# Performance work log

Hardware: AMD Instinct MI355X
Metric: run time of the kernel (lower is better)

## Reference

```python
import jax, jax.numpy as jnp
import numpy as np

RES = 512
STEPS = 128
SIGMA = 0.01


def _sample_cubic(curves, t):
    # curves: [N,4,2], t: [S] in [0,1]. De Casteljau, matching the torch module.
    p0, p1, p2, p3 = curves[:, 0], curves[:, 1], curves[:, 2], curves[:, 3]  # each [N,2]

    def lerp(a, b):  # [N,2] -> [N,2,S]
        return a[:, :, None] + (b - a)[:, :, None] * t

    a01, a12, a23 = lerp(p0, p1), lerp(p1, p2), lerp(p2, p3)
    qa = a01 + t * (a12 - a01)   # quadratic over first 3 points
    qb = a12 + t * (a23 - a12)   # quadratic over last 3 points
    curve = qa + t * (qb - qa)   # cubic, [N,2,S]
    # torch.cat([...], dim=1) over curves of shape [2,S] -> [2, N*S]
    return jnp.moveaxis(curve, 0, 1).reshape(2, -1)


def setup_inputs() -> dict:
    key = jax.random.key(0)
    curves = jax.random.uniform(key, (8, 4, 2), dtype=jnp.float32)
    return {"curves": curves}


def reference(curves) -> jnp.ndarray:
    t = jnp.linspace(0.0, 1.0, STEPS)
    curve = _sample_cubic(curves, t)  # [2, T], T = N*STEPS
    x, y = curve[0], curve[1]
    grid = jnp.arange(RES, dtype=curve.dtype) / RES  # pixel coords / res
    inv = 1.0 / (2.0 * SIGMA * SIGMA)
    # exp(-(dx^2+dy^2)/2s^2) factors exactly: raster[a,b] = sum_s Ex[a,s]*Ey[b,s]
    Ex = jnp.exp(-(x[None, :] - grid[:, None]) ** 2 * inv)  # [RES, T]
    Ey = jnp.exp(-(y[None, :] - grid[:, None]) ** 2 * inv)  # [RES, T]
    raster = Ex @ Ey.T  # [RES, RES], raster[a,b]
    # torch returns transpose(raster, 0, 1)
    return raster.T
```

## Files before the change

### kernel.cpp

```cpp
#include <hip/hip_runtime.h>


constexpr int RES_   = 512;
constexpr int TILE   = 64;
constexpr int KSPLIT = 8;
constexpr int KB     = 1024 / KSPLIT;
constexpr int KC     = 64;

__global__ __launch_bounds__(256)
void bezier_partial(const float* __restrict__ curves, float* __restrict__ part) {
    __shared__ float xs[KB], ys[KB];
    __shared__ float ex_s[KC][TILE];
    __shared__ float ey_s[KC][TILE];

    const int tid   = threadIdx.x;
    const int ibase = blockIdx.x * TILE;
    const int jbase = blockIdx.y * TILE;
    const int kbase = blockIdx.z * KB;

    if (tid < KB) {
        int p = kbase + tid;
        int c = p >> 7;
        float t = (float)(p & 127) * (1.0f / 127.0f);
        const float* cp = curves + c * 8;
        float p0x = cp[0], p0y = cp[1];
        float p1x = cp[2], p1y = cp[3];
        float p2x = cp[4], p2y = cp[5];
        float p3x = cp[6], p3y = cp[7];
        float a01x = p0x + (p1x - p0x) * t, a01y = p0y + (p1y - p0y) * t;
        float a12x = p1x + (p2x - p1x) * t, a12y = p1y + (p2y - p1y) * t;
        float a23x = p2x + (p3x - p2x) * t, a23y = p2y + (p3y - p2y) * t;
        float qax = a01x + (a12x - a01x) * t, qay = a01y + (a12y - a01y) * t;
        float qbx = a12x + (a23x - a12x) * t, qby = a12y + (a23y - a12y) * t;
        xs[tid] = qax + (qbx - qax) * t;
        ys[tid] = qay + (qby - qay) * t;
    }
    __syncthreads();

    const int it = tid & 15, jt = tid >> 4;
    const int ib = it * 4, jb = jt * 4;
    float acc[4][4];
#pragma unroll
    for (int r = 0; r < 4; ++r)
#pragma unroll
        for (int c = 0; c < 4; ++c) acc[r][c] = 0.0f;

    for (int chunk = 0; chunk < KB / KC; ++chunk) {
#pragma unroll
        for (int e = 0; e < (KC * TILE) / 256; ++e) {
            int idx = e * 256 + tid;
            int kk  = idx >> 6;
            int ii  = idx & 63;
            float xv = xs[chunk * KC + kk];
            float yv = ys[chunk * KC + kk];
            float dx = xv - (float)(ibase + ii) * (1.0f / 512.0f);
            float dy = yv - (float)(jbase + ii) * (1.0f / 512.0f);
            ex_s[kk][ii] = __expf(dx * dx * (-5000.0f));
            ey_s[kk][ii] = __expf(dy * dy * (-5000.0f));
        }
        __syncthreads();

#pragma unroll 4
        for (int kk = 0; kk < KC; ++kk) {
            const float4 a = *reinterpret_cast<const float4*>(&ex_s[kk][ib]);
            const float4 b = *reinterpret_cast<const float4*>(&ey_s[kk][jb]);
            acc[0][0] += b.x * a.x; acc[0][1] += b.x * a.y;
            acc[0][2] += b.x * a.z; acc[0][3] += b.x * a.w;
            acc[1][0] += b.y * a.x; acc[1][1] += b.y * a.y;
            acc[1][2] += b.y * a.z; acc[1][3] += b.y * a.w;
            acc[2][0] += b.z * a.x; acc[2][1] += b.z * a.y;
            acc[2][2] += b.z * a.z; acc[2][3] += b.z * a.w;
            acc[3][0] += b.w * a.x; acc[3][1] += b.w * a.y;
            acc[3][2] += b.w * a.z; acc[3][3] += b.w * a.w;
        }
        __syncthreads();
    }

    float* slice = part + (size_t)blockIdx.z * (RES_ * RES_);
#pragma unroll
    for (int r = 0; r < 4; ++r) {
        int j = jbase + jb + r;
        float4 v = make_float4(acc[r][0], acc[r][1], acc[r][2], acc[r][3]);
        *reinterpret_cast<float4*>(&slice[j * RES_ + ibase + ib]) = v;
    }
}

__global__ __launch_bounds__(256)
void reduce_k(const float* __restrict__ part, float* __restrict__ out) {
    int i = blockIdx.x * blockDim.x + threadIdx.x;
    const float4* p4 = reinterpret_cast<const float4*>(part);
    float4 s = p4[i];
#pragma unroll
    for (int z = 1; z < KSPLIT; ++z) {
        float4 v = p4[(size_t)z * (RES_ * RES_ / 4) + i];
        s.x += v.x; s.y += v.y; s.z += v.z; s.w += v.w;
    }
    reinterpret_cast<float4*>(out)[i] = s;
}

extern "C" void kernel_launch(void* const* d_in, const int* in_sizes, int n_in,
                              void* d_out, int out_size, void* d_ws, size_t ws_size,
                              hipStream_t stream) {
    const float* curves = (const float*)d_in[0];
    float* out  = (float*)d_out;
    float* part = (float*)d_ws;

    dim3 grid(RES_ / TILE, RES_ / TILE, KSPLIT);
    bezier_partial<<<grid, dim3(256), 0, stream>>>(curves, part);

    reduce_k<<<dim3(RES_ * RES_ / 4 / 256), dim3(256), 0, stream>>>(part, out);
}
```

Baseline: 67.44 us.

## Use 128x128 tiles with 8x8 register blocking and 16-way K split

Each block now covers a 128x128 output tile, and each thread accumulates an 8x8 register tile instead of 4x4. The K split rises from 8 to 16, so each block handles 64 samples. All exp factors for those samples are computed once into shared memory, which drops the chunk loop and its extra barriers. This raises arithmetic intensity per shared-memory load, but it doubles the partial-sum buffer written by the first kernel and read by the reduction. It also halves the block count and needs 16 slices of workspace.

```diff
diff --git a/kernel.cpp b/kernel.cpp
--- a/kernel.cpp
+++ b/kernel.cpp
@@ -2,16 +2,15 @@
 
 
 constexpr int RES_   = 512;
-constexpr int TILE   = 64;
-constexpr int KSPLIT = 8;
+constexpr int TILE   = 128;
+constexpr int KSPLIT = 16;
 constexpr int KB     = 1024 / KSPLIT;
-constexpr int KC     = 64;
 
 __global__ __launch_bounds__(256)
 void bezier_partial(const float* __restrict__ curves, float* __restrict__ part) {
     __shared__ float xs[KB], ys[KB];
-    __shared__ float ex_s[KC][TILE];
-    __shared__ float ey_s[KC][TILE];
+    __shared__ float ex_s[KB][TILE];
+    __shared__ float ey_s[KB][TILE];
 
     const int tid   = threadIdx.x;
     const int ibase = blockIdx.x * TILE;
@@ -37,51 +36,50 @@
     }
     __syncthreads();
 
+#pragma unroll
+    for (int e = 0; e < (KB * TILE) / 256; ++e) {
+        int idx = e * 256 + tid;
+        int kk  = idx >> 7;
+        int ii  = idx & 127;
+        float xv = xs[kk];
+        float yv = ys[kk];
+        float dx = xv - (float)(ibase + ii) * (1.0f / 512.0f);
+        float dy = yv - (float)(jbase + ii) * (1.0f / 512.0f);
+        ex_s[kk][ii] = __expf(dx * dx * (-5000.0f));
+        ey_s[kk][ii] = __expf(dy * dy * (-5000.0f));
+    }
+    __syncthreads();
+
     const int it = tid & 15, jt = tid >> 4;
-    const int ib = it * 4, jb = jt * 4;
-    float acc[4][4];
+    const int ib = it * 8, jb = jt * 8;
+    float acc[8][8];
 #pragma unroll
-    for (int r = 0; r < 4; ++r)
+    for (int r = 0; r < 8; ++r)
 #pragma unroll
-        for (int c = 0; c < 4; ++c) acc[r][c] = 0.0f;
+        for (int c = 0; c < 8; ++c) acc[r][c] = 0.0f;
 
-    for (int chunk = 0; chunk < KB / KC; ++chunk) {
+#pragma unroll 2
+    for (int kk = 0; kk < KB; ++kk) {
+        const float4 a0 = *reinterpret_cast<const float4*>(&ex_s[kk][ib]);
+        const float4 a1 = *reinterpret_cast<const float4*>(&ex_s[kk][ib + 4]);
+        const float4 b0 = *reinterpret_cast<const float4*>(&ey_s[kk][jb]);
+        const float4 b1 = *reinterpret_cast<const float4*>(&ey_s[kk][jb + 4]);
+        const float av[8] = {a0.x, a0.y, a0.z, a0.w, a1.x, a1.y, a1.z, a1.w};
+        const float bv[8] = {b0.x, b0.y, b0.z, b0.w, b1.x, b1.y, b1.z, b1.w};
 #pragma unroll
-        for (int e = 0; e < (KC * TILE) / 256; ++e) {
-            int idx = e * 256 + tid;
-            int kk  = idx >> 6;
-            int ii  = idx & 63;
-            float xv = xs[chunk * KC + kk];
-            float yv = ys[chunk * KC + kk];
-            float dx = xv - (float)(ibase + ii) * (1.0f / 512.0f);
-            float dy = yv - (float)(jbase + ii) * (1.0f / 512.0f);
-            ex_s[kk][ii] = __expf(dx * dx * (-5000.0f));
-            ey_s[kk][ii] = __expf(dy * dy * (-5000.0f));
-        }
-        __syncthreads();
-
-#pragma unroll 4
-        for (int kk = 0; kk < KC; ++kk) {
-            const float4 a = *reinterpret_cast<const float4*>(&ex_s[kk][ib]);
-            const float4 b = *reinterpret_cast<const float4*>(&ey_s[kk][jb]);
-            acc[0][0] += b.x * a.x; acc[0][1] += b.x * a.y;
-            acc[0][2] += b.x * a.z; acc[0][3] += b.x * a.w;
-            acc[1][0] += b.y * a.x; acc[1][1] += b.y * a.y;
-            acc[1][2] += b.y * a.z; acc[1][3] += b.y * a.w;
-            acc[2][0] += b.z * a.x; acc[2][1] += b.z * a.y;
-            acc[2][2] += b.z * a.z; acc[2][3] += b.z * a.w;
-            acc[3][0] += b.w * a.x; acc[3][1] += b.w * a.y;
-            acc[3][2] += b.w * a.z; acc[3][3] += b.w * a.w;
-        }
-        __syncthreads();
+        for (int r = 0; r < 8; ++r)
+#pragma unroll
+            for (int c = 0; c < 8; ++c)
+                acc[r][c] += bv[r] * av[c];
     }
 
     float* slice = part + (size_t)blockIdx.z * (RES_ * RES_);
 #pragma unroll
-    for (int r = 0; r < 4; ++r) {
+    for (int r = 0; r < 8; ++r) {
         int j = jbase + jb + r;
-        float4 v = make_float4(acc[r][0], acc[r][1], acc[r][2], acc[r][3]);
-        *reinterpret_cast<float4*>(&slice[j * RES_ + ibase + ib]) = v;
+        float* row = &slice[j * RES_ + ibase + ib];
+        *reinterpret_cast<float4*>(row)     = make_float4(acc[r][0], acc[r][1], acc[r][2], acc[r][3]);
+        *reinterpret_cast<float4*>(row + 4) = make_float4(acc[r][4], acc[r][5], acc[r][6], acc[r][7]);
     }
 }
 
```

Result: slower. 73.63 us (+9.2%).

## Fuse split-K reduction into main kernel via last-block ticket counter

Applied to the files above, without the earlier changes.

Removes the separate reduction kernel. Each block writes its partial tile to a tile-contiguous workspace, then bumps a per-tile atomic ticket, and the last of the KSPLIT blocks sums the partials and writes the output tile. The Gaussian table fill is also vectorised so each thread computes four exps and does float4 shared stores. This trades a kernel launch and a full-image partial pass for a memset, threadfences and an atomic, and the final reduction now runs on only 64 blocks.

```diff
diff --git a/kernel.cpp b/kernel.cpp
--- a/kernel.cpp
+++ b/kernel.cpp
@@ -6,17 +6,21 @@
 constexpr int KSPLIT = 8;
 constexpr int KB     = 1024 / KSPLIT;
 constexpr int KC     = 64;
+constexpr int NTX    = RES_ / TILE;
 
 __global__ __launch_bounds__(256)
-void bezier_partial(const float* __restrict__ curves, float* __restrict__ part) {
+void bezier_fused(const float* __restrict__ curves, float* __restrict__ out,
+                  unsigned int* __restrict__ tickets, float* __restrict__ part) {
     __shared__ float xs[KB], ys[KB];
-    __shared__ float ex_s[KC][TILE];
-    __shared__ float ey_s[KC][TILE];
+    __shared__ __align__(16) float ex_s[KC][TILE];
+    __shared__ __align__(16) float ey_s[KC][TILE];
+    __shared__ unsigned int s_old;
 
-    const int tid   = threadIdx.x;
-    const int ibase = blockIdx.x * TILE;
-    const int jbase = blockIdx.y * TILE;
-    const int kbase = blockIdx.z * KB;
+    const int tid     = threadIdx.x;
+    const int ibase   = blockIdx.x * TILE;
+    const int jbase   = blockIdx.y * TILE;
+    const int tile_id = blockIdx.y * NTX + blockIdx.x;
+    const int kbase   = blockIdx.z * KB;
 
     if (tid < KB) {
         int p = kbase + tid;
@@ -47,16 +51,27 @@
 
     for (int chunk = 0; chunk < KB / KC; ++chunk) {
 #pragma unroll
-        for (int e = 0; e < (KC * TILE) / 256; ++e) {
-            int idx = e * 256 + tid;
-            int kk  = idx >> 6;
-            int ii  = idx & 63;
+        for (int e = 0; e < (KC * TILE) / (256 * 4); ++e) {
+            int idx4 = (e * 256 + tid) * 4;
+            int kk   = idx4 >> 6;
+            int ii   = idx4 & 63;
             float xv = xs[chunk * KC + kk];
             float yv = ys[chunk * KC + kk];
-            float dx = xv - (float)(ibase + ii) * (1.0f / 512.0f);
-            float dy = yv - (float)(jbase + ii) * (1.0f / 512.0f);
-            ex_s[kk][ii] = __expf(dx * dx * (-5000.0f));
-            ey_s[kk][ii] = __expf(dy * dy * (-5000.0f));
+            float g0 = (float)(ibase + ii) * (1.0f / 512.0f);
+            float h0 = (float)(jbase + ii) * (1.0f / 512.0f);
+            float4 vx, vy;
+            {
+                float d0 = xv - g0, d1 = xv - (g0 + 1.0f/512.0f),
+                      d2 = xv - (g0 + 2.0f/512.0f), d3 = xv - (g0 + 3.0f/512.0f);
+                vx = make_float4(__expf(d0*d0*-5000.0f), __expf(d1*d1*-5000.0f),
+                                 __expf(d2*d2*-5000.0f), __expf(d3*d3*-5000.0f));
+                float e0 = yv - h0, e1 = yv - (h0 + 1.0f/512.0f),
+                      e2 = yv - (h0 + 2.0f/512.0f), e3 = yv - (h0 + 3.0f/512.0f);
+                vy = make_float4(__expf(e0*e0*-5000.0f), __expf(e1*e1*-5000.0f),
+                                 __expf(e2*e2*-5000.0f), __expf(e3*e3*-5000.0f));
+            }
+            *reinterpret_cast<float4*>(&ex_s[kk][ii]) = vx;
+            *reinterpret_cast<float4*>(&ey_s[kk][ii]) = vy;
         }
         __syncthreads();
 
@@ -76,37 +91,50 @@
         __syncthreads();
     }
 
-    float* slice = part + (size_t)blockIdx.z * (RES_ * RES_);
+    float* pt = part + ((size_t)tile_id * KSPLIT + blockIdx.z) * (TILE * TILE);
 #pragma unroll
     for (int r = 0; r < 4; ++r) {
-        int j = jbase + jb + r;
-        float4 v = make_float4(acc[r][0], acc[r][1], acc[r][2], acc[r][3]);
-        *reinterpret_cast<float4*>(&slice[j * RES_ + ibase + ib]) = v;
+        *reinterpret_cast<float4*>(&pt[(jb + r) * TILE + ib]) =
+            make_float4(acc[r][0], acc[r][1], acc[r][2], acc[r][3]);
     }
-}
 
-__global__ __launch_bounds__(256)
-void reduce_k(const float* __restrict__ part, float* __restrict__ out) {
-    int i = blockIdx.x * blockDim.x + threadIdx.x;
-    const float4* p4 = reinterpret_cast<const float4*>(part);
-    float4 s = p4[i];
+    __threadfence();
+    __syncthreads();
+    if (tid == 0) s_old = atomicAdd(&tickets[tile_id], 1u);
+    __syncthreads();
+
+    if (s_old == KSPLIT - 1) {
+        __threadfence();
+        const float4* p4 = reinterpret_cast<const float4*>(
+            part + (size_t)tile_id * KSPLIT * (TILE * TILE));
 #pragma unroll
-    for (int z = 1; z < KSPLIT; ++z) {
-        float4 v = p4[(size_t)z * (RES_ * RES_ / 4) + i];
-        s.x += v.x; s.y += v.y; s.z += v.z; s.w += v.w;
+        for (int e = 0; e < (TILE * TILE) / (256 * 4); ++e) {
+            int idx = e * 256 + tid;
+            float4 s = p4[idx];
+#pragma unroll
+            for (int z = 1; z < KSPLIT; ++z) {
+                float4 v = p4[z * (TILE * TILE / 4) + idx];
+                s.x += v.x; s.y += v.y; s.z += v.z; s.w += v.w;
+            }
+            int fi   = idx * 4;
+            int j_in = fi >> 6;
+            int i_in = fi & 63;
+            *reinterpret_cast<float4*>(&out[(jbase + j_in) * RES_ + ibase + i_in]) = s;
+        }
     }
-    reinterpret_cast<float4*>(out)[i] = s;
 }
 
 extern "C" void kernel_launch(void* const* d_in, const int* in_sizes, int n_in,
                               void* d_out, int out_size, void* d_ws, size_t ws_size,
                               hipStream_t stream) {
     const float* curves = (const float*)d_in[0];
-    float* out  = (float*)d_out;
-    float* part = (float*)d_ws;
+    float* out = (float*)d_out;
 
-    dim3 grid(RES_ / TILE, RES_ / TILE, KSPLIT);
-    bezier_partial<<<grid, dim3(256), 0, stream>>>(curves, part);
+    unsigned int* tickets = (unsigned int*)d_ws;
+    float* part = (float*)((char*)d_ws + 4096);
 
-    reduce_k<<<dim3(RES_ * RES_ / 4 / 256), dim3(256), 0, stream>>>(part, out);
+    hipMemsetAsync(tickets, 0, (RES_ / TILE) * (RES_ / TILE) * sizeof(unsigned int), stream);
+
+    dim3 grid(NTX, NTX, KSPLIT);
+    bezier_fused<<<grid, dim3(256), 0, stream>>>(curves, out, tickets, part);
 }
```

Result: slower. 115.4 us (+71.2%).
